# Kernel optimization log

Measured on AMD Instinct MI355X. Metric: run time of the kernel, lower is better.

## Reference

```python
import jax, jax.numpy as jnp
import numpy as np

H = 64  # GRU hidden size (hard-coded in module)


def _gru_scan(x_proj, w_hh, b_hh):
    """Run a single-direction GRU (torch gate order r,z,n).

    x_proj: [T, B, 3H] precomputed input projections (x @ W_ih^T + b_ih)
    w_hh:   [3H, H], b_hh: [3H]
    Returns all hidden states [T, B, H].
    """
    w_hr, w_hz, w_hn = w_hh[:H], w_hh[H:2 * H], w_hh[2 * H:]
    b_hr, b_hz, b_hn = b_hh[:H], b_hh[H:2 * H], b_hh[2 * H:]
    B = x_proj.shape[1]
    h0 = jnp.zeros((B, H), dtype=x_proj.dtype)

    def step(h, xp):
        xr, xz, xn = xp[:, :H], xp[:, H:2 * H], xp[:, 2 * H:]
        r = jax.nn.sigmoid(xr + h @ w_hr.T + b_hr)
        z = jax.nn.sigmoid(xz + h @ w_hz.T + b_hz)
        n = jnp.tanh(xn + r * (h @ w_hn.T + b_hn))
        h_new = (1.0 - z) * n + z * h
        return h_new, h_new

    _, hs = jax.lax.scan(step, h0, x_proj)
    return hs  # [T, B, H]


def setup_inputs() -> dict:
    key = jax.random.key(0)
    ks = jax.random.split(key, 11)
    B, T, D = 512, 512, 32
    s_ih = 1.0 / np.sqrt(H)
    u = lambda k, shape: jax.random.uniform(k, shape, jnp.float32, -s_ih, s_ih)
    return {
        "x": jax.random.normal(ks[0], (B, T, D), dtype=jnp.float32),
        # forward direction GRU params
        "w_ih_f": u(ks[1], (3 * H, D)),
        "w_hh_f": u(ks[2], (3 * H, H)),
        "b_ih_f": u(ks[3], (3 * H,)),
        "b_hh_f": u(ks[4], (3 * H,)),
        # backward direction GRU params
        "w_ih_b": u(ks[5], (3 * H, D)),
        "w_hh_b": u(ks[6], (3 * H, H)),
        "b_ih_b": u(ks[7], (3 * H,)),
        "b_hh_b": u(ks[8], (3 * H,)),
        # fc head: Linear(128,64) -> LeakyReLU(0.2) -> Linear(64,1)
        "fc1_w": jax.random.normal(ks[9], (64, 2 * H), dtype=jnp.float32) * (1.0 / np.sqrt(2 * H)),
        "fc1_b": jnp.zeros((64,), dtype=jnp.float32),
        "fc2_w": jax.random.normal(ks[10], (1, 64), dtype=jnp.float32) * (1.0 / np.sqrt(64)),
        "fc2_b": jnp.zeros((1,), dtype=jnp.float32),
    }


def reference(x, w_ih_f, w_hh_f, b_ih_f, b_hh_f,
              w_ih_b, w_hh_b, b_ih_b, b_hh_b,
              fc1_w, fc1_b, fc2_w, fc2_b):
    # x: [B, T, D] -> time-major [T, B, D]
    xt = jnp.swapaxes(x, 0, 1)
    # precompute input projections for all timesteps (one big GEMM per dir)
    xp_f = jnp.einsum('tbd,gd->tbg', xt, w_ih_f) + b_ih_f  # [T,B,3H]
    xp_b = jnp.einsum('tbd,gd->tbg', xt, w_ih_b) + b_ih_b

    hs_f = _gru_scan(xp_f, w_hh_f, b_hh_f)            # forward over t=0..T-1
    hs_b = _gru_scan(xp_b[::-1], w_hh_b, b_hh_b)      # backward: reversed time
    # out[:, -1, :] = concat(fwd hidden at t=T-1, bwd hidden at t=T-1).
    # bwd hidden at original t=T-1 is the FIRST step of the reversed scan.
    last = jnp.concatenate([hs_f[-1], hs_b[0]], axis=-1)  # [B, 2H]

    h1 = last @ fc1_w.T + fc1_b
    h1 = jnp.where(h1 >= 0, h1, 0.2 * h1)  # LeakyReLU(0.2)
    return h1 @ fc2_w.T + fc2_b  # [B, 1]
```

## Files before the change

kernel.cpp:

```cpp
#include <hip/hip_runtime.h>

namespace {
constexpr int T = 512;
constexpr int BATCH = 512;
constexpr int D = 32;
constexpr int H = 64;
constexpr int THREADS = 256;
}

typedef float v2f __attribute__((ext_vector_type(2)));

__device__ __forceinline__ float rcpf(float x) { return __builtin_amdgcn_rcpf(x); }
__device__ __forceinline__ float sigm(float x) { return rcpf(1.0f + __expf(-x)); }
__device__ __forceinline__ float tanh_fast(float x) {
    return 1.0f - 2.0f * rcpf(__expf(2.0f * x) + 1.0f);
}

__device__ __forceinline__ void pk2(v2f& acc, v2f w, v2f v) {
    asm("v_pk_fma_f32 %0, %1, %2, %0" : "+v"(acc) : "v"(w), "v"(v));
}

__device__ __forceinline__ float quad_sum(float v) {
    int i = __builtin_bit_cast(int, v);
    float t = __builtin_bit_cast(float,
        __builtin_amdgcn_update_dpp(0, i, 0xB1, 0xF, 0xF, true));
    v += t;
    i = __builtin_bit_cast(int, v);
    t = __builtin_bit_cast(float,
        __builtin_amdgcn_update_dpp(0, i, 0x4E, 0xF, 0xF, true));
    return v + t;
}

__global__ __launch_bounds__(THREADS) void gru_fused_kernel(
    const float* __restrict__ x,
    const float* __restrict__ w_ih_f, const float* __restrict__ w_hh_f,
    const float* __restrict__ b_ih_f, const float* __restrict__ b_hh_f,
    const float* __restrict__ w_ih_b, const float* __restrict__ b_ih_b,
    const float* __restrict__ b_hh_b,
    const float* __restrict__ fc1_w, const float* __restrict__ fc1_b,
    const float* __restrict__ fc2_w, const float* __restrict__ fc2_b,
    float* __restrict__ out)
{
    const int b   = blockIdx.x;
    const int tid = threadIdx.x;
    const int j   = tid >> 2;
    const int q   = tid & 3;
    const int kh0 = q * 16;
    const int kx0 = q * 8;

    __shared__ v2f x_lds[T * D / 2];
    __shared__ __align__(16) float h_lds[2][H];
    __shared__ float last_lds[2 * H];

    v2f wr2[8], wz2[8], wn2[8], ur2[4], uz2[4], un2[4];
    {
        const v2f* pr = reinterpret_cast<const v2f*>(w_hh_f + (size_t)j * H + kh0);
        const v2f* pz = reinterpret_cast<const v2f*>(w_hh_f + (size_t)(H + j) * H + kh0);
        const v2f* pn = reinterpret_cast<const v2f*>(w_hh_f + (size_t)(2 * H + j) * H + kh0);
        #pragma unroll
        for (int m = 0; m < 8; ++m) { wr2[m] = pr[m]; wz2[m] = pz[m]; wn2[m] = pn[m]; }
        const v2f* qr = reinterpret_cast<const v2f*>(w_ih_f + (size_t)j * D + kx0);
        const v2f* qz = reinterpret_cast<const v2f*>(w_ih_f + (size_t)(H + j) * D + kx0);
        const v2f* qn = reinterpret_cast<const v2f*>(w_ih_f + (size_t)(2 * H + j) * D + kx0);
        #pragma unroll
        for (int m = 0; m < 4; ++m) { ur2[m] = qr[m]; uz2[m] = qz[m]; un2[m] = qn[m]; }
    }

    const float pre_r  = b_ih_f[j]         + b_hh_f[j];
    const float pre_z  = b_ih_f[H + j]     + b_hh_f[H + j];
    const float pre_nx = b_ih_f[2 * H + j];
    const float pre_nh = b_hh_f[2 * H + j];

    {
        const float4* xg  = reinterpret_cast<const float4*>(x + (size_t)b * T * D);
        float4*       xl4 = reinterpret_cast<float4*>(x_lds);
        #pragma unroll 4
        for (int i = tid; i < T * D / 4; i += THREADS) xl4[i] = xg[i];
    }
    if (tid < H) h_lds[0][tid] = 0.0f;
    __syncthreads();

    v2f axr = {0.f, 0.f}, axz = {0.f, 0.f};
    float vnx;
    {
        const v2f* xt2 = x_lds + q * 4;
        v2f x0 = xt2[0], x1 = xt2[1], x2 = xt2[2], x3 = xt2[3];
        v2f axn = {0.f, 0.f};
        pk2(axr, ur2[0], x0); pk2(axr, ur2[1], x1); pk2(axr, ur2[2], x2); pk2(axr, ur2[3], x3);
        pk2(axz, uz2[0], x0); pk2(axz, uz2[1], x1); pk2(axz, uz2[2], x2); pk2(axz, uz2[3], x3);
        pk2(axn, un2[0], x0); pk2(axn, un2[1], x1); pk2(axn, un2[2], x2); pk2(axn, un2[3], x3);
        vnx = quad_sum(axn.x + axn.y);
    }

    float hold = 0.0f;

    for (int t = 0; t < T; ++t) {
        const int cur = t & 1, nxt = cur ^ 1;

        v2f hh[8];
        {
            const v2f* hp = reinterpret_cast<const v2f*>(&h_lds[cur][kh0]);
            #pragma unroll
            for (int m = 0; m < 8; ++m) hh[m] = hp[m];
        }

        v2f pr = axr, pz = axz, nh = {0.f, 0.f};
        #pragma unroll
        for (int m = 0; m < 8; ++m) pk2(pr, wr2[m], hh[m]);
        #pragma unroll
        for (int m = 0; m < 8; ++m) pk2(pz, wz2[m], hh[m]);
        #pragma unroll
        for (int m = 0; m < 8; ++m) pk2(nh, wn2[m], hh[m]);

        const float vr  = quad_sum(pr.x + pr.y);
        const float vz  = quad_sum(pz.x + pz.y);
        const float vnh = quad_sum(nh.x + nh.y);

        const float r = sigm(vr + pre_r);
        const float z = sigm(vz + pre_z);
        const float n = tanh_fast(vnx + pre_nx + r * (vnh + pre_nh));
        const float hnew = n + z * (hold - n);
        hold = hnew;
        if (q == 0) h_lds[nxt][j] = hnew;

        {
            const int tn = (t + 1) & (T - 1);
            const v2f* xt2 = x_lds + tn * 16 + q * 4;
            v2f x0 = xt2[0], x1 = xt2[1], x2 = xt2[2], x3 = xt2[3];
            axr = {0.f, 0.f}; axz = {0.f, 0.f};
            v2f axn = {0.f, 0.f};
            pk2(axr, ur2[0], x0); pk2(axr, ur2[1], x1); pk2(axr, ur2[2], x2); pk2(axr, ur2[3], x3);
            pk2(axz, uz2[0], x0); pk2(axz, uz2[1], x1); pk2(axz, uz2[2], x2); pk2(axz, uz2[3], x3);
            pk2(axn, un2[0], x0); pk2(axn, un2[1], x1); pk2(axn, un2[2], x2); pk2(axn, un2[3], x3);
            vnx = quad_sum(axn.x + axn.y);
        }

        __syncthreads();
    }

    const int wave = tid >> 6, lane = tid & 63;

    if (wave == 0) last_lds[lane] = h_lds[T & 1][lane];

    if (wave == 1) {
        const float* xT = reinterpret_cast<const float*>(x_lds) + (T - 1) * D;
        const int jj = lane;
        float xr = b_ih_b[jj];
        float xz = b_ih_b[H + jj];
        float xn = b_ih_b[2 * H + jj];
        #pragma unroll
        for (int k = 0; k < D; ++k) {
            const float xv = xT[k];
            xr = fmaf(w_ih_b[(size_t)jj * D + k],           xv, xr);
            xz = fmaf(w_ih_b[(size_t)(H + jj) * D + k],     xv, xz);
            xn = fmaf(w_ih_b[(size_t)(2 * H + jj) * D + k], xv, xn);
        }
        const float r = sigm(xr + b_hh_b[jj]);
        const float z = sigm(xz + b_hh_b[H + jj]);
        const float n = tanh_fast(xn + r * b_hh_b[2 * H + jj]);
        last_lds[H + jj] = (1.0f - z) * n;
    }
    __syncthreads();

    if (wave == 0) {
        float acc = fc1_b[lane];
        const float* w1 = fc1_w + (size_t)lane * (2 * H);
        #pragma unroll 8
        for (int c = 0; c < 2 * H; ++c) acc = fmaf(w1[c], last_lds[c], acc);
        acc = (acc >= 0.0f) ? acc : 0.2f * acc;
        float red = acc * fc2_w[lane];
        #pragma unroll
        for (int off = 32; off > 0; off >>= 1)
            red += __shfl_down(red, off);
        if (lane == 0) out[b] = red + fc2_b[0];
    }
}

extern "C" void kernel_launch(void* const* d_in, const int* in_sizes, int n_in,
                              void* d_out, int out_size, void* d_ws, size_t ws_size,
                              hipStream_t stream) {
    const float* x      = (const float*)d_in[0];
    const float* w_ih_f = (const float*)d_in[1];
    const float* w_hh_f = (const float*)d_in[2];
    const float* b_ih_f = (const float*)d_in[3];
    const float* b_hh_f = (const float*)d_in[4];
    const float* w_ih_b = (const float*)d_in[5];
    const float* b_ih_b = (const float*)d_in[7];
    const float* b_hh_b = (const float*)d_in[8];
    const float* fc1_w  = (const float*)d_in[9];
    const float* fc1_b  = (const float*)d_in[10];
    const float* fc2_w  = (const float*)d_in[11];
    const float* fc2_b  = (const float*)d_in[12];
    float* out = (float*)d_out;

    gru_fused_kernel<<<BATCH, THREADS, 0, stream>>>(
        x, w_ih_f, w_hh_f, b_ih_f, b_hh_f,
        w_ih_b, b_ih_b, b_hh_b,
        fc1_w, fc1_b, fc2_w, fc2_b, out);
}
```

Baseline: 209.7 us.

## Stream x from global with register prefetch instead of staging in LDS

Removes the 64 KB LDS staging buffer for the input sequence. Each thread now loads its x slice from global memory two timesteps ahead into registers, and computes the input projection for t+1 inside the current step, interleaved with the recurrent FMAs. This cuts the upfront bulk copy and barrier, and the drop in LDS use could let more blocks share a CU. In exchange, every step now issues a global load whose latency must be hidden within one recurrence step.

Measured after the change: 236.3 us. +12.7%, slower.

```diff
diff --git a/kernel.cpp b/kernel.cpp
--- a/kernel.cpp
+++ b/kernel.cpp
@@ -48,7 +48,6 @@
     const int kh0 = q * 16;
     const int kx0 = q * 8;
 
-    __shared__ v2f x_lds[T * D / 2];
     __shared__ __align__(16) float h_lds[2][H];
     __shared__ float last_lds[2 * H];
 
@@ -71,26 +70,25 @@
     const float pre_nx = b_ih_f[2 * H + j];
     const float pre_nh = b_hh_f[2 * H + j];
 
+    const float* xrow = x + (size_t)b * T * D;
+
+    if (tid < H) h_lds[0][tid] = 0.0f;
+
+    v2f axr = {0.f, 0.f}, axz = {0.f, 0.f}, axn = {0.f, 0.f};
     {
-        const float4* xg  = reinterpret_cast<const float4*>(x + (size_t)b * T * D);
-        float4*       xl4 = reinterpret_cast<float4*>(x_lds);
-        #pragma unroll 4
-        for (int i = tid; i < T * D / 4; i += THREADS) xl4[i] = xg[i];
-    }
-    if (tid < H) h_lds[0][tid] = 0.0f;
-    __syncthreads();
-
-    v2f axr = {0.f, 0.f}, axz = {0.f, 0.f};
-    float vnx;
-    {
-        const v2f* xt2 = x_lds + q * 4;
-        v2f x0 = xt2[0], x1 = xt2[1], x2 = xt2[2], x3 = xt2[3];
-        v2f axn = {0.f, 0.f};
+        const v2f* px = reinterpret_cast<const v2f*>(xrow + kx0);
+        v2f x0 = px[0], x1 = px[1], x2 = px[2], x3 = px[3];
         pk2(axr, ur2[0], x0); pk2(axr, ur2[1], x1); pk2(axr, ur2[2], x2); pk2(axr, ur2[3], x3);
         pk2(axz, uz2[0], x0); pk2(axz, uz2[1], x1); pk2(axz, uz2[2], x2); pk2(axz, uz2[3], x3);
         pk2(axn, un2[0], x0); pk2(axn, un2[1], x1); pk2(axn, un2[2], x2); pk2(axn, un2[3], x3);
-        vnx = quad_sum(axn.x + axn.y);
     }
+    v2f nx0, nx1, nx2, nx3;
+    {
+        const v2f* px = reinterpret_cast<const v2f*>(xrow + D + kx0);
+        nx0 = px[0]; nx1 = px[1]; nx2 = px[2]; nx3 = px[3];
+    }
+
+    __syncthreads();
 
     float hold = 0.0f;
 
@@ -111,10 +109,23 @@
         for (int m = 0; m < 8; ++m) pk2(pz, wz2[m], hh[m]);
         #pragma unroll
         for (int m = 0; m < 8; ++m) pk2(nh, wn2[m], hh[m]);
+        const v2f axn_t = axn;
+
+        axr = {0.f, 0.f}; axz = {0.f, 0.f}; axn = {0.f, 0.f};
+        pk2(axr, ur2[0], nx0); pk2(axr, ur2[1], nx1); pk2(axr, ur2[2], nx2); pk2(axr, ur2[3], nx3);
+        pk2(axz, uz2[0], nx0); pk2(axz, uz2[1], nx1); pk2(axz, uz2[2], nx2); pk2(axz, uz2[3], nx3);
+        pk2(axn, un2[0], nx0); pk2(axn, un2[1], nx1); pk2(axn, un2[2], nx2); pk2(axn, un2[3], nx3);
+
+        {
+            const v2f* px = reinterpret_cast<const v2f*>(
+                xrow + ((t + 2) & (T - 1)) * D + kx0);
+            nx0 = px[0]; nx1 = px[1]; nx2 = px[2]; nx3 = px[3];
+        }
 
         const float vr  = quad_sum(pr.x + pr.y);
         const float vz  = quad_sum(pz.x + pz.y);
         const float vnh = quad_sum(nh.x + nh.y);
+        const float vnx = quad_sum(axn_t.x + axn_t.y);
 
         const float r = sigm(vr + pre_r);
         const float z = sigm(vz + pre_z);
@@ -122,19 +133,6 @@
         const float hnew = n + z * (hold - n);
         hold = hnew;
         if (q == 0) h_lds[nxt][j] = hnew;
-
-        {
-            const int tn = (t + 1) & (T - 1);
-            const v2f* xt2 = x_lds + tn * 16 + q * 4;
-            v2f x0 = xt2[0], x1 = xt2[1], x2 = xt2[2], x3 = xt2[3];
-            axr = {0.f, 0.f}; axz = {0.f, 0.f};
-            v2f axn = {0.f, 0.f};
-            pk2(axr, ur2[0], x0); pk2(axr, ur2[1], x1); pk2(axr, ur2[2], x2); pk2(axr, ur2[3], x3);
-            pk2(axz, uz2[0], x0); pk2(axz, uz2[1], x1); pk2(axz, uz2[2], x2); pk2(axz, uz2[3], x3);
-            pk2(axn, un2[0], x0); pk2(axn, un2[1], x1); pk2(axn, un2[2], x2); pk2(axn, un2[3], x3);
-            vnx = quad_sum(axn.x + axn.y);
-        }
-
         __syncthreads();
     }
 
@@ -143,7 +141,7 @@
     if (wave == 0) last_lds[lane] = h_lds[T & 1][lane];
 
     if (wave == 1) {
-        const float* xT = reinterpret_cast<const float*>(x_lds) + (T - 1) * D;
+        const float* xT = xrow + (size_t)(T - 1) * D;
         const int jj = lane;
         float xr = b_ih_b[jj];
         float xz = b_ih_b[H + jj];
```
